# Kernel tuning notes

Measured on AMD Instinct MI355X. Metric: run time of the kernel, lower is better.

Reference implementation:

```python
import jax, jax.numpy as jnp
import numpy as np
import itertools

B, T, C, H = 2, 2048, 1024, 8
HD = C // H  # head_dim = 128


def _head_dirs():
    # 8 trigrams = vertices of cube {-1,+1}^3, L2-normalized (norm sqrt(3))
    signs = [-1.0, 1.0]
    tri = np.array(list(itertools.product(signs, repeat=3)), dtype=np.float32)
    tri = tri / np.linalg.norm(tri, axis=1, keepdims=True)
    return jnp.asarray(tri[:H])  # [H, 3]


def setup_inputs() -> dict:
    key = jax.random.key(0)
    ks = jax.random.split(key, 5)
    w = lambda k, sh: jax.random.normal(k, sh, dtype=jnp.float32) * 0.02
    return {
        "x": jax.random.normal(ks[0], (B, T, C), dtype=jnp.float32),
        "Wq": w(ks[1], (H * 3, C)),
        "Wk": w(ks[2], (H * 3, C)),
        "Wv": w(ks[3], (C, C)),
        "Wo": w(ks[4], (C, C)),
        "scale": jnp.asarray(1.0 / np.sqrt(3.0), dtype=jnp.float32),
    }


def reference(x, Wq, Wk, Wv, Wo, scale):
    Bb, Tt, Cc = x.shape
    dirs = _head_dirs()  # [H, 3] constant buffer
    # tiny 3-dim per-head Q/K projections
    q3 = (x @ Wq.T).reshape(Bb, Tt, H, 3).transpose(0, 2, 1, 3)  # [B,H,T,3]
    k3 = (x @ Wk.T).reshape(Bb, Tt, H, 3).transpose(0, 2, 1, 3)  # [B,H,T,3]
    v = (x @ Wv.T).reshape(Bb, Tt, H, HD).transpose(0, 2, 1, 3)  # [B,H,T,HD]
    # projections of q/k onto each head's trigram direction
    q_on_dir = jnp.einsum('bhtd,hd->bht', q3, dirs)  # [B,H,T]
    k_on_dir = jnp.einsum('bhtd,hd->bht', k3, dirs)  # [B,H,T]
    # scores = scaled 3-dim dot product + geometric outer-product bias
    scores = jnp.einsum('bhtd,bhsd->bhts', q3, k3) * scale \
        + q_on_dir[..., :, None] * k_on_dir[..., None, :]  # [B,H,T,T]
    causal = jnp.tril(jnp.ones((Tt, Tt), dtype=bool))
    scores = jnp.where(causal, scores, -jnp.inf)
    attn = jax.nn.softmax(scores, axis=-1)
    out = jnp.einsum('bhts,bhsd->bhtd', attn, v)  # [B,H,T,HD]
    out = out.transpose(0, 2, 1, 3).reshape(Bb, Tt, Cc)
    return out @ Wo.T
```

## Files before the change

### kernel.cpp

```cpp
#include <hip/hip_runtime.h>
#include <hip/hip_bf16.h>

#define B_  2
#define T_  2048
#define C_  1024
#define H_  8
#define HD_ 128
#define M_  (B_*T_)

typedef short  bf16x8 __attribute__((ext_vector_type(8)));
typedef float  f32x4  __attribute__((ext_vector_type(4)));
typedef unsigned short u16x8 __attribute__((ext_vector_type(8)));

typedef const __attribute__((address_space(1))) void* gas_ptr;
typedef __attribute__((address_space(3))) void*       las_ptr;

#define L2E_ 1.4426950408889634f

static __device__ __forceinline__ unsigned short f2bf(float f) {
    unsigned int u = __float_as_uint(f);
    u += 0x7fffu + ((u >> 16) & 1u);
    return (unsigned short)(u >> 16);
}
static __device__ __forceinline__ float bf2f(unsigned short u) {
    return __uint_as_float(((unsigned int)u) << 16);
}
static __device__ __forceinline__ float exp2_fast(float x) {
#if __has_builtin(__builtin_amdgcn_exp2f)
    return __builtin_amdgcn_exp2f(x);
#else
    return exp2f(x);
#endif
}

__global__ __launch_bounds__(256) void k_convert_w(const float* __restrict__ Wv,
                                                   const float* __restrict__ Wo,
                                                   unsigned short* __restrict__ wvbf,
                                                   unsigned short* __restrict__ wobf) {
    int i = blockIdx.x * 256 + threadIdx.x;
    const float* src; unsigned short* dst; int off;
    if (i < 262144) { src = Wv; dst = wvbf; off = i; }
    else            { src = Wo; dst = wobf; off = i - 262144; }
    float4 v = reinterpret_cast<const float4*>(src)[off];
    ushort4 o;
    o.x = f2bf(v.x); o.y = f2bf(v.y); o.z = f2bf(v.z); o.w = f2bf(v.w);
    reinterpret_cast<ushort4*>(dst)[off] = o;
}

__global__ __launch_bounds__(256) void k_proj_qk(const float* __restrict__ x,
                                                 const float* __restrict__ Wq,
                                                 const float* __restrict__ Wk,
                                                 const float* __restrict__ scale_p,
                                                 float* __restrict__ qt,
                                                 float* __restrict__ kt,
                                                 unsigned short* __restrict__ xbf) {
    __shared__ __align__(16) float wl[48][260];
    __shared__ __align__(16) float xl[16][260];
    __shared__ float res[16][48];
    const int tid  = threadIdx.x;
    const int row0 = blockIdx.x << 4;
    const int r    = tid >> 4, sub = tid & 15;
    float a0 = 0.f, a1 = 0.f, a2 = 0.f;

    for (int ch = 0; ch < 4; ++ch) {
        const int k0 = ch * 256;
        #pragma unroll
        for (int i = 0; i < 12; ++i) {
            int fi = i * 256 + tid;
            int wr = fi >> 6, wc = (fi & 63) * 4;
            const float* src = (wr < 24) ? (Wq + (size_t)wr * C_) : (Wk + (size_t)(wr - 24) * C_);
            *reinterpret_cast<float4*>(&wl[wr][wc]) = *reinterpret_cast<const float4*>(src + k0 + wc);
        }
        #pragma unroll
        for (int i = 0; i < 4; ++i) {
            int fi = i * 256 + tid;
            int xr = fi >> 6, xc = (fi & 63) * 4;
            size_t goff = (size_t)(row0 + xr) * C_ + k0 + xc;
            float4 xv = *reinterpret_cast<const float4*>(x + goff);
            *reinterpret_cast<float4*>(&xl[xr][xc]) = xv;
            ushort4 o;
            o.x = f2bf(xv.x); o.y = f2bf(xv.y); o.z = f2bf(xv.z); o.w = f2bf(xv.w);
            *reinterpret_cast<ushort4*>(xbf + goff) = o;
        }
        __syncthreads();
        const int oc = sub * 3;
        #pragma unroll 4
        for (int k = 0; k < 256; k += 4) {
            float4 xv = *reinterpret_cast<const float4*>(&xl[r][k]);
            float4 w0 = *reinterpret_cast<const float4*>(&wl[oc + 0][k]);
            float4 w1 = *reinterpret_cast<const float4*>(&wl[oc + 1][k]);
            float4 w2 = *reinterpret_cast<const float4*>(&wl[oc + 2][k]);
            a0 += xv.x * w0.x + xv.y * w0.y + xv.z * w0.z + xv.w * w0.w;
            a1 += xv.x * w1.x + xv.y * w1.y + xv.z * w1.z + xv.w * w1.w;
            a2 += xv.x * w2.x + xv.y * w2.y + xv.z * w2.z + xv.w * w2.w;
        }
        __syncthreads();
    }
    res[r][sub * 3 + 0] = a0;
    res[r][sub * 3 + 1] = a1;
    res[r][sub * 3 + 2] = a2;
    __syncthreads();

    {
        const int rr = tid >> 4, s2 = tid & 15;
        const int isK = s2 >> 3, h = s2 & 7;
        const float r3 = 0.57735026918962576f;
        float d0 = (h & 4) ? r3 : -r3;
        float d1 = (h & 2) ? r3 : -r3;
        float d2 = (h & 1) ? r3 : -r3;
        const float* v3 = &res[rr][isK * 24 + h * 3];
        float a = v3[0], b = v3[1], c = v3[2];
        float ond = a * d0 + b * d1 + c * d2;
        float sc = scale_p[0];
        float4 ov = isK ? make_float4(a, b, c, ond)
                        : make_float4(a * sc * L2E_, b * sc * L2E_, c * sc * L2E_, ond * L2E_);
        float* dst = isK ? kt : qt;
        int grow = row0 + rr;
        int b_ = grow >> 11, t_idx = grow & (T_ - 1);
        reinterpret_cast<float4*>(dst)[(size_t)(b_ * H_ + h) * T_ + t_idx] = ov;
    }
}

template <int MODE>
__global__ __launch_bounds__(256) void k_gemm128x64(const unsigned short* __restrict__ A,
                                                    const unsigned short* __restrict__ Bw,
                                                    void* __restrict__ Cout,
                                                    int Mdim, int Ndim, int Kdim) {
    __shared__ __align__(16) unsigned short lds_a[8][128][8];
    __shared__ __align__(16) unsigned short lds_b[8][64][8];
    const int tid = threadIdx.x;
    const int nbn = Ndim >> 6;
    const int bm = (blockIdx.x / nbn) << 7;
    const int bn = (blockIdx.x % nbn) << 6;
    const int w = tid >> 6, l = tid & 63;
    const int wm = (w >> 1) << 6, wn = (w & 1) << 5;
    const int lh = l & 15, lq = l >> 4;

    f32x4 acc[4][2];
    #pragma unroll
    for (int i = 0; i < 4; ++i)
        #pragma unroll
        for (int j = 0; j < 2; ++j)
            acc[i][j] = (f32x4){0.f, 0.f, 0.f, 0.f};

    for (int k0 = 0; k0 < Kdim; k0 += 64) {
        #pragma unroll
        for (int p = 0; p < 4; ++p) {
            int flat = p * 256 + tid;
            int kq = flat >> 7, row = flat & 127;
            __builtin_amdgcn_global_load_lds((gas_ptr)(A + (size_t)(bm + row) * Kdim + k0 + kq * 8),
                (las_ptr)(&lds_a[0][0][0] + (size_t)flat * 8), 16, 0, 0);
        }
        #pragma unroll
        for (int p = 0; p < 2; ++p) {
            int flat = p * 256 + tid;
            int kq = flat >> 6, row = flat & 63;
            __builtin_amdgcn_global_load_lds((gas_ptr)(Bw + (size_t)(bn + row) * Kdim + k0 + kq * 8),
                (las_ptr)(&lds_b[0][0][0] + (size_t)flat * 8), 16, 0, 0);
        }
        __syncthreads();

        #pragma unroll
        for (int kk = 0; kk < 2; ++kk) {
            bf16x8 af[4], bfr[2];
            #pragma unroll
            for (int f = 0; f < 4; ++f)
                af[f] = *reinterpret_cast<const bf16x8*>(&lds_a[lq + 4 * kk][wm + f * 16 + lh][0]);
            #pragma unroll
            for (int f = 0; f < 2; ++f)
                bfr[f] = *reinterpret_cast<const bf16x8*>(&lds_b[lq + 4 * kk][wn + f * 16 + lh][0]);
            #pragma unroll
            for (int i = 0; i < 4; ++i)
                #pragma unroll
                for (int j = 0; j < 2; ++j)
                    acc[i][j] = __builtin_amdgcn_mfma_f32_16x16x32_bf16(af[i], bfr[j], acc[i][j], 0, 0, 0);
        }
        __syncthreads();
    }

    if constexpr (MODE == 0) {
        float* Cf = (float*)Cout;
        #pragma unroll
        for (int i = 0; i < 4; ++i) {
            int rbase = bm + wm + i * 16 + lq * 4;
            #pragma unroll
            for (int j = 0; j < 2; ++j) {
                int cidx = bn + wn + j * 16 + lh;
                #pragma unroll
                for (int r = 0; r < 4; ++r)
                    Cf[(size_t)(rbase + r) * Ndim + cidx] = acc[i][j][r];
            }
        }
    } else {
        __shared__ unsigned short ldsT[128][72];
        #pragma unroll
        for (int i = 0; i < 4; ++i)
            #pragma unroll
            for (int j = 0; j < 2; ++j)
                #pragma unroll
                for (int r = 0; r < 4; ++r)
                    ldsT[wm + i * 16 + lq * 4 + r][wn + j * 16 + lh] = f2bf(acc[i][j][r]);
        __syncthreads();
        unsigned short* vt_out = (unsigned short*)Cout;
        int c = tid & 63, part = tid >> 6;
        int b = bm >> 11, t0 = bm & (T_ - 1);
        unsigned short* dst = vt_out + ((size_t)b * C_ + bn + c) * T_ + t0 + part * 32;
        #pragma unroll
        for (int jj = 0; jj < 4; ++jj) {
            u16x8 v;
            #pragma unroll
            for (int k = 0; k < 8; ++k) v[k] = ldsT[part * 32 + jj * 8 + k][c];
            *reinterpret_cast<u16x8*>(dst + jj * 8) = v;
        }
    }
}

__global__ __launch_bounds__(256) void k_attn_lds(
        const float4* __restrict__ qt, const float4* __restrict__ kt,
        const unsigned short* __restrict__ vt,
        unsigned short* __restrict__ mpart,
        float2* __restrict__ mlbuf,
        int nsp, int lg2nsp) {
    __shared__ __align__(16) unsigned short lv[2][4096];
    const int tid = threadIdx.x;
    const int w = tid >> 6, l = tid & 63;
    const int lh = l & 15, lg = l >> 4;
    const int bid = blockIdx.x;
    const int qb = 31 - (bid >> (4 + lg2nsp));
    const int sp = (bid >> 4) & (nsp - 1);
    const int bh = bid & 15;
    const int q0 = qb << 6;
    const int qrow = q0 + 4 * lh + w;
    const int nt = 2 * qb + 2;

    const float4* qtb = qt + (size_t)bh * T_;
    const float4* ktb = kt + (size_t)bh * T_;
    const unsigned short* vtb = vt + (size_t)bh * HD_ * T_;

    const int flatA = tid, flatB = 256 + tid;
    const unsigned short* srcA = vtb + (size_t)(((flatA >> 6) << 4) | (flatA & 15)) * T_ + ((flatA >> 4) & 3) * 8;
    const unsigned short* srcB = vtb + (size_t)(((flatB >> 6) << 4) | (flatB & 15)) * T_ + ((flatB >> 4) & 3) * 8;

#define STAGE_V(ST, BUF) do {                                                  \
    int s0e_ = (ST) << 5;                                                      \
    __builtin_amdgcn_global_load_lds((gas_ptr)(srcA + s0e_),                   \
        (las_ptr)(&lv[BUF][0] + (size_t)flatA * 8), 16, 0, 0);                 \
    __builtin_amdgcn_global_load_lds((gas_ptr)(srcB + s0e_),                   \
        (las_ptr)(&lv[BUF][0] + (size_t)flatB * 8), 16, 0, 0);                 \
} while (0)

    const float4 q4 = qtb[qrow];
    f32x4 acc[8];
    #pragma unroll
    for (int n = 0; n < 8; ++n) acc[n] = (f32x4){0.f, 0.f, 0.f, 0.f};
    float m = -1e30f, lsum = 0.f;

    if (sp < nt) STAGE_V(sp, 0);
    __syncthreads();

    int buf = 0;
    for (int st = sp; st < nt; st += nsp) {
        if (st + nsp < nt) STAGE_V(st + nsp, buf ^ 1);

        const int s0 = st << 5;
        const int sbase = s0 + lg * 8;

        float p[8];
        float mt = -1e30f;
        #pragma unroll
        for (int jj = 0; jj < 8; ++jj) {
            float4 k4 = ktb[sbase + jj];
            float sc = fmaf(q4.x, k4.x, fmaf(q4.y, k4.y, fmaf(q4.z, k4.z, q4.w * k4.w)));
            sc = (sbase + jj > qrow) ? -1e30f : sc;
            p[jj] = sc;
            mt = fmaxf(mt, sc);
        }
        mt = fmaxf(mt, __shfl_xor(mt, 16));
        mt = fmaxf(mt, __shfl_xor(mt, 32));
        if (__any(mt > m + 8.f)) {
            float mnew = fmaxf(m, mt);
            float corr = exp2_fast(m - mnew);
            m = mnew;
            lsum *= corr;
            float c0 = __shfl(corr, 4 * lg + 0);
            float c1 = __shfl(corr, 4 * lg + 1);
            float c2 = __shfl(corr, 4 * lg + 2);
            float c3 = __shfl(corr, 4 * lg + 3);
            #pragma unroll
            for (int n = 0; n < 8; ++n) {
                acc[n][0] *= c0; acc[n][1] *= c1; acc[n][2] *= c2; acc[n][3] *= c3;
            }
        }
        float ps = 0.f;
        #pragma unroll
        for (int jj = 0; jj < 8; ++jj) {
            float e = exp2_fast(p[jj] - m);
            e = (sbase + jj > qrow) ? 0.f : e;
            p[jj] = e;
            ps += e;
        }
        ps += __shfl_xor(ps, 16);
        ps += __shfl_xor(ps, 32);
        lsum += ps;

        bf16x8 pa;
        #pragma unroll
        for (int jj = 0; jj < 8; ++jj) pa[jj] = (short)f2bf(p[jj]);

        #pragma unroll
        for (int n = 0; n < 8; ++n) {
            bf16x8 vf = *reinterpret_cast<const bf16x8*>(&lv[buf][(size_t)(n * 64 + lg * 16 + lh) * 8]);
            acc[n] = __builtin_amdgcn_mfma_f32_16x16x32_bf16(pa, vf, acc[n], 0, 0, 0);
        }

        __syncthreads();
        buf ^= 1;
    }
#undef STAGE_V

    unsigned short* mp = mpart + (size_t)(sp * 16 + bh) * T_ * HD_;
    #pragma unroll
    for (int n = 0; n < 8; ++n) {
        #pragma unroll
        for (int r = 0; r < 4; ++r) {
            int row = q0 + 16 * lg + 4 * r + w;
            mp[(size_t)row * HD_ + n * 16 + lh] = f2bf(acc[n][r]);
        }
    }
    if (lg == 0)
        mlbuf[(size_t)(sp * 16 + bh) * T_ + qrow] = make_float2(m, lsum);
}

__global__ __launch_bounds__(256) void k_combine(const unsigned short* __restrict__ mpart,
                                                 const float2* __restrict__ mlbuf,
                                                 unsigned short* __restrict__ attnbf,
                                                 int nsp) {
    int idx = blockIdx.x * 256 + threadIdx.x;
    int bh = idx >> 16;
    int rem = idx & 65535;
    int t = rem >> 5, d0 = (rem & 31) * 4;
    float mg = -1e30f, den = 0.f;
    float ax = 0.f, ay = 0.f, az = 0.f, aw = 0.f;
    for (int s = 0; s < nsp; ++s) {
        float2 ml = mlbuf[(size_t)(s * 16 + bh) * T_ + t];
        ushort4 a = *reinterpret_cast<const ushort4*>(
            mpart + ((size_t)(s * 16 + bh) * T_ + t) * HD_ + d0);
        float mn = fmaxf(mg, ml.x);
        float cOld = exp2_fast(mg - mn);
        float cNew = exp2_fast(ml.x - mn);
        den = den * cOld + ml.y * cNew;
        ax = ax * cOld + bf2f(a.x) * cNew;
        ay = ay * cOld + bf2f(a.y) * cNew;
        az = az * cOld + bf2f(a.z) * cNew;
        aw = aw * cOld + bf2f(a.w) * cNew;
        mg = mn;
    }
    float inv = 1.f / den;
    int b = bh >> 3, h = bh & 7;
    ushort4 o;
    o.x = f2bf(ax * inv); o.y = f2bf(ay * inv);
    o.z = f2bf(az * inv); o.w = f2bf(aw * inv);
    *reinterpret_cast<ushort4*>(attnbf + ((size_t)(b * T_ + t) * C_ + h * HD_ + d0)) = o;
}

extern "C" void kernel_launch(void* const* d_in, const int* in_sizes, int n_in,
                              void* d_out, int out_size, void* d_ws, size_t ws_size,
                              hipStream_t stream) {
    const float* x     = (const float*)d_in[0];
    const float* Wq    = (const float*)d_in[1];
    const float* Wk    = (const float*)d_in[2];
    const float* Wv    = (const float*)d_in[3];
    const float* Wo    = (const float*)d_in[4];
    const float* scale = (const float*)d_in[5];
    float* out = (float*)d_out;

    int nsp, lg2nsp;
    if (ws_size >= 82837504)      { nsp = 8; lg2nsp = 3; }
    else if (ws_size >= 46137344) { nsp = 4; lg2nsp = 2; }
    else                          { nsp = 2; lg2nsp = 1; }

    char* ws = (char*)d_ws;
    size_t o = (size_t)nsp * 8388608;
    unsigned short* mpart  = (unsigned short*)(ws);
    unsigned short* xbf    = (unsigned short*)(ws);
    unsigned short* wvbf   = (unsigned short*)(ws + 8388608);
    float*          qt     = (float*)(ws + o);
    float*          kt     = (float*)(ws + o + 524288);
    unsigned short* vt     = (unsigned short*)(ws + o + 1048576);
    unsigned short* attnbf = (unsigned short*)(ws + o + 1048576);
    unsigned short* wobf   = (unsigned short*)(ws + o + 9437184);
    float2*         mlbuf  = (float2*)(ws + o + 11534336);

    k_convert_w<<<2048, 256, 0, stream>>>(Wv, Wo, wvbf, wobf);

    k_proj_qk<<<M_ / 16, 256, 0, stream>>>(x, Wq, Wk, scale, qt, kt, xbf);

    k_gemm128x64<2><<<(M_ / 128) * (C_ / 64), 256, 0, stream>>>(xbf, wvbf, (void*)vt, M_, C_, C_);

    k_attn_lds<<<32 * nsp * 16, 256, 0, stream>>>(
        reinterpret_cast<const float4*>(qt), reinterpret_cast<const float4*>(kt), vt,
        mpart, mlbuf, nsp, lg2nsp);

    k_combine<<<4096, 256, 0, stream>>>(mpart, mlbuf, attnbf, nsp);

    k_gemm128x64<0><<<(M_ / 128) * (C_ / 64), 256, 0, stream>>>(attnbf, wobf, (void*)out, M_, C_, C_);
}
```

Before: 153.9 us.

## Use per-query-block variable split count to balance causal attention work

```diff
diff --git a/kernel.cpp b/kernel.cpp
--- a/kernel.cpp
+++ b/kernel.cpp
@@ -16,6 +16,7 @@
 typedef __attribute__((address_space(3))) void*       las_ptr;
 
 #define L2E_ 1.4426950408889634f
+#define NSPMAX_ 7
 
 static __device__ __forceinline__ unsigned short f2bf(float f) {
     unsigned int u = __float_as_uint(f);
@@ -219,16 +220,22 @@
         const float4* __restrict__ qt, const float4* __restrict__ kt,
         const unsigned short* __restrict__ vt,
         unsigned short* __restrict__ mpart,
-        float2* __restrict__ mlbuf,
-        int nsp, int lg2nsp) {
+        float2* __restrict__ mlbuf) {
     __shared__ __align__(16) unsigned short lv[2][4096];
     const int tid = threadIdx.x;
     const int w = tid >> 6, l = tid & 63;
     const int lh = l & 15, lg = l >> 4;
-    const int bid = blockIdx.x;
-    const int qb = 31 - (bid >> (4 + lg2nsp));
-    const int sp = (bid >> 4) & (nsp - 1);
-    const int bh = bid & 15;
+
+    int rem = blockIdx.x, qb = 0, ns = 1;
+    #pragma unroll 1
+    for (int q = 31; q >= 0; --q) {
+        int s = (q + 5) / 5;
+        int c = s << 4;
+        if (rem < c) { qb = q; ns = s; break; }
+        rem -= c;
+    }
+    const int sp = rem >> 4;
+    const int bh = rem & 15;
     const int q0 = qb << 6;
     const int qrow = q0 + 4 * lh + w;
     const int nt = 2 * qb + 2;
@@ -259,8 +266,8 @@
     __syncthreads();
 
     int buf = 0;
-    for (int st = sp; st < nt; st += nsp) {
-        if (st + nsp < nt) STAGE_V(st + nsp, buf ^ 1);
+    for (int st = sp; st < nt; st += ns) {
+        if (st + ns < nt) STAGE_V(st + ns, buf ^ 1);
 
         const int s0 = st << 5;
         const int sbase = s0 + lg * 8;
@@ -333,15 +340,15 @@
 
 __global__ __launch_bounds__(256) void k_combine(const unsigned short* __restrict__ mpart,
                                                  const float2* __restrict__ mlbuf,
-                                                 unsigned short* __restrict__ attnbf,
-                                                 int nsp) {
+                                                 unsigned short* __restrict__ attnbf) {
     int idx = blockIdx.x * 256 + threadIdx.x;
     int bh = idx >> 16;
     int rem = idx & 65535;
     int t = rem >> 5, d0 = (rem & 31) * 4;
+    const int ns = ((t >> 6) + 5) / 5;
     float mg = -1e30f, den = 0.f;
     float ax = 0.f, ay = 0.f, az = 0.f, aw = 0.f;
-    for (int s = 0; s < nsp; ++s) {
+    for (int s = 0; s < ns; ++s) {
         float2 ml = mlbuf[(size_t)(s * 16 + bh) * T_ + t];
         ushort4 a = *reinterpret_cast<const ushort4*>(
             mpart + ((size_t)(s * 16 + bh) * T_ + t) * HD_ + d0);
@@ -374,13 +381,8 @@
     const float* scale = (const float*)d_in[5];
     float* out = (float*)d_out;
 
-    int nsp, lg2nsp;
-    if (ws_size >= 82837504)      { nsp = 8; lg2nsp = 3; }
-    else if (ws_size >= 46137344) { nsp = 4; lg2nsp = 2; }
-    else                          { nsp = 2; lg2nsp = 1; }
-
     char* ws = (char*)d_ws;
-    size_t o = (size_t)nsp * 8388608;
+    size_t o = (size_t)NSPMAX_ * 8388608;
     unsigned short* mpart  = (unsigned short*)(ws);
     unsigned short* xbf    = (unsigned short*)(ws);
     unsigned short* wvbf   = (unsigned short*)(ws + 8388608);
@@ -397,11 +399,11 @@
 
     k_gemm128x64<2><<<(M_ / 128) * (C_ / 64), 256, 0, stream>>>(xbf, wvbf, (void*)vt, M_, C_, C_);
 
-    k_attn_lds<<<32 * nsp * 16, 256, 0, stream>>>(
+    k_attn_lds<<<1904, 256, 0, stream>>>(
         reinterpret_cast<const float4*>(qt), reinterpret_cast<const float4*>(kt), vt,
-        mpart, mlbuf, nsp, lg2nsp);
-
-    k_combine<<<4096, 256, 0, stream>>>(mpart, mlbuf, attnbf, nsp);
+        mpart, mlbuf);
+
+    k_combine<<<4096, 256, 0, stream>>>(mpart, mlbuf, attnbf);
 
     k_gemm128x64<0><<<(M_ / 128) * (C_ / 64), 256, 0, stream>>>(attnbf, wobf, (void*)out, M_, C_, C_);
 }
```

New measurement: 150.0 us. 2.5% less time.
